# Performance work log

Measured on AMD Instinct MI355X. Metric: run time of the kernel, lower is better.

Reference implementation:

```python
import jax, jax.numpy as jnp
import numpy as np
import math

D_MODEL = 1024
N_HEADS = 16
HEAD_DIM = D_MODEL // N_HEADS
SEQ_LEN = 8192
INCLUDE_LOCAL = 2


def get_dilated_positions(seq_len, include_local=2):
    # Faithful numpy port of the torch pattern generator (runs once at setup).
    max_attend = include_local + int(math.ceil(math.log2(seq_len + 1)))
    positions = np.zeros((seq_len, max_attend), dtype=np.int64)
    mask = np.zeros((seq_len, max_attend), dtype=bool)
    for i in range(seq_len):
        ap = [i]
        for j in range(1, include_local + 1):
            if i - j >= 0:
                ap.append(i - j)
        k = 2
        while i - 2 ** k >= 0:
            ap.append(i - 2 ** k)
            k += 1
        positions[i, :len(ap)] = ap
        mask[i, :len(ap)] = True
    return positions, mask


def setup_inputs() -> dict:
    key = jax.random.key(0)
    kx, kq, kk, kv, ko = jax.random.split(key, 5)
    x = jax.random.normal(kx, (1, SEQ_LEN, D_MODEL), dtype=jnp.float32)
    # nn.Linear(bias=False) weights, torch layout [out_features, in_features]
    s = 0.02
    q_w = jax.random.normal(kq, (D_MODEL, D_MODEL), dtype=jnp.float32) * s
    k_w = jax.random.normal(kk, (D_MODEL, D_MODEL), dtype=jnp.float32) * s
    v_w = jax.random.normal(kv, (D_MODEL, D_MODEL), dtype=jnp.float32) * s
    o_w = jax.random.normal(ko, (D_MODEL, D_MODEL), dtype=jnp.float32) * s
    pos_np, mask_np = get_dilated_positions(SEQ_LEN, INCLUDE_LOCAL)
    return {
        "x": x,
        "q_w": q_w, "k_w": k_w, "v_w": v_w, "o_w": o_w,
        "positions": jnp.asarray(pos_np),   # (S, A) int64 indices
        "attend_mask": jnp.asarray(mask_np) # (S, A) bool
    }


def reference(x, q_w, k_w, v_w, o_w, positions, attend_mask):
    B, S, _ = x.shape
    H, Dh = N_HEADS, HEAD_DIM
    scale = Dh ** -0.5

    q = (x @ q_w.T).reshape(B, S, H, Dh).transpose(0, 2, 1, 3)  # (B,H,S,Dh)
    k = (x @ k_w.T).reshape(B, S, H, Dh).transpose(0, 2, 1, 3)
    v = (x @ v_w.T).reshape(B, S, H, Dh).transpose(0, 2, 1, 3)

    # Gather K/V at the dilated positions: (B,H,S,A,Dh)
    k_sparse = k[:, :, positions, :]
    v_sparse = v[:, :, positions, :]

    scores = jnp.einsum('bhsd,bhsad->bhsa', q, k_sparse) * scale
    scores = jnp.where(attend_mask[None, None, :, :], scores, -jnp.inf)
    attn = jax.nn.softmax(scores, axis=-1)  # dropout p in eval / 0.0 -> identity

    out = jnp.einsum('bhsa,bhsad->bhsd', attn, v_sparse)
    out = out.transpose(0, 2, 1, 3).reshape(B, S, D_MODEL)
    return out @ o_w.T
```

## Files before the change

### kernel.cpp

```cpp
#include <hip/hip_runtime.h>
#include <hip/hip_bf16.h>

typedef __bf16 bf16_t;
typedef __bf16 bf16x4 __attribute__((ext_vector_type(4)));
typedef __bf16 bf16x8 __attribute__((ext_vector_type(8)));
typedef float floatx16 __attribute__((ext_vector_type(16)));

#define SEQ    8192
#define DM     1024
#define NHEADS 16
#define HDIM   64

__device__ __forceinline__ void async_ld16(bf16_t* lds, const bf16_t* g) {
  __builtin_amdgcn_global_load_lds(
      (__attribute__((address_space(1))) void*)g,
      (__attribute__((address_space(3))) void*)lds, 16, 0, 0);
}

__global__ __launch_bounds__(256)
void cvt_all(const float* __restrict__ x,  const float* __restrict__ qw,
             const float* __restrict__ kw, const float* __restrict__ vw,
             const float* __restrict__ ow,
             bf16_t* __restrict__ Xb,  bf16_t* __restrict__ QWb,
             bf16_t* __restrict__ KWb, bf16_t* __restrict__ VWb,
             bf16_t* __restrict__ OWb) {
  const int b = blockIdx.x;
  const float* in; bf16_t* out; int g;
  if (b < 8192) { in = x; out = Xb; g = b; }
  else {
    const int w  = (b - 8192) >> 10;
    const int wb = (b - 8192) & 1023;
    switch (w) {
      case 0:  in = qw; out = QWb; break;
      case 1:  in = kw; out = KWb; break;
      case 2:  in = vw; out = VWb; break;
      default: in = ow; out = OWb; break;
    }
    g = wb;
  }
  const int idx = (g * 256 + threadIdx.x) * 4;
  float4 v = *(const float4*)(in + idx);
  bf16x4 o = { (bf16_t)v.x, (bf16_t)v.y, (bf16_t)v.z, (bf16_t)v.w };
  *(bf16x4*)(out + idx) = o;
}

template <typename OutT>
__device__ __forceinline__ void gemm128_core(
    const bf16_t* __restrict__ A, const bf16_t* __restrict__ B,
    OutT* __restrict__ C, float scl)
{
  constexpr int Kdim = DM;
  __shared__ __attribute__((aligned(16))) bf16_t sA[128 * 64];
  __shared__ __attribute__((aligned(16))) bf16_t sB[128 * 64];

  const int tid  = threadIdx.x;
  const int wave = tid >> 6;
  const int lane = tid & 63;
  const int l31  = lane & 31;
  const int half = lane >> 5;
  const int wr   = (wave >> 1) * 64;
  const int wc   = (wave & 1) * 64;

  const int gc = (lane & 7) ^ ((lane >> 3) & 7);
  const size_t arow0 = (size_t)blockIdx.x * 128 + wave * 32 + (lane >> 3);
  const size_t brow0 = (size_t)blockIdx.y * 128 + wave * 32 + (lane >> 3);
  const bf16_t* Ag = A + arow0 * Kdim + gc * 8;
  const bf16_t* Bg = B + brow0 * Kdim + gc * 8;
  bf16_t* sAw = sA + wave * 32 * 64;
  bf16_t* sBw = sB + wave * 32 * 64;

  floatx16 acc[2][2];
  #pragma unroll
  for (int i = 0; i < 2; ++i)
    #pragma unroll
    for (int j = 0; j < 2; ++j)
      acc[i][j] = (floatx16)(0.0f);

  const int sw = l31 & 7;

  for (int ko = 0; ko < Kdim; ko += 64) {
    #pragma unroll
    for (int n = 0; n < 4; ++n) {
      async_ld16(sAw + n * 512, Ag + (size_t)n * 8 * Kdim + ko);
      async_ld16(sBw + n * 512, Bg + (size_t)n * 8 * Kdim + ko);
    }
    __syncthreads();

    #pragma unroll
    for (int s = 0; s < 4; ++s) {
      const int ck   = s * 2 + half;
      const int slot = (ck ^ sw) * 8;
      bf16x8 af[2], bfr[2];
      #pragma unroll
      for (int mi = 0; mi < 2; ++mi)
        af[mi] = *(const bf16x8*)&sA[(wr + mi * 32 + l31) * 64 + slot];
      #pragma unroll
      for (int ni = 0; ni < 2; ++ni)
        bfr[ni] = *(const bf16x8*)&sB[(wc + ni * 32 + l31) * 64 + slot];

      #pragma unroll
      for (int mi = 0; mi < 2; ++mi)
        #pragma unroll
        for (int ni = 0; ni < 2; ++ni)
          acc[mi][ni] = __builtin_amdgcn_mfma_f32_32x32x16_bf16(af[mi], bfr[ni], acc[mi][ni], 0, 0, 0);
    }

    __syncthreads();
  }

  const int crow0 = blockIdx.x * 128 + wr + 4 * half;
  const int ccol0 = blockIdx.y * 128 + wc + l31;
  #pragma unroll
  for (int mi = 0; mi < 2; ++mi)
    #pragma unroll
    for (int ni = 0; ni < 2; ++ni)
      #pragma unroll
      for (int r = 0; r < 16; ++r) {
        const int row = crow0 + mi * 32 + (r & 3) + 8 * (r >> 2);
        C[(size_t)row * DM + (ccol0 + ni * 32)] = (OutT)(acc[mi][ni][r] * scl);
      }
}

__global__ __launch_bounds__(256)
void gemm_proj(const bf16_t* __restrict__ A, const bf16_t* __restrict__ B,
               bf16_t* __restrict__ C, float scl)
{
  gemm128_core<bf16_t>(A, B, C, scl);
}

__global__ __launch_bounds__(256)
void gemm_outk(const bf16_t* __restrict__ A, const bf16_t* __restrict__ B,
               float* __restrict__ C)
{
  gemm128_core<float>(A, B, C, 1.0f);
}

__global__ __launch_bounds__(256)
void dilated_attn(const bf16_t* __restrict__ Q, const bf16_t* __restrict__ K,
                  const bf16_t* __restrict__ V, bf16_t* O)
{
  const int lane = threadIdx.x & 63;
  const int wv   = threadIdx.x >> 6;
  const int bid  = blockIdx.x;
  const int jj   = bid >> 3;
  const int chunk= (bid & 7) + ((jj >> 6) << 3);
  const int i    = chunk * 256 + (jj & 63) * 4 + wv;
  const size_t base = (size_t)i * DM + lane * 16;

  bf16x8 q0 = *(const bf16x8*)(Q + base);
  bf16x8 q1 = *(const bf16x8*)(Q + base + 8);
  float qf[16];
  #pragma unroll
  for (int j = 0; j < 8; ++j) { qf[j] = (float)q0[j]; qf[j + 8] = (float)q1[j]; }

  const int npos = (i == 0) ? 1 : (33 - __builtin_clz((unsigned)i));
  auto pos_addr = [&](int t) -> size_t {
    const int off = (t == 0) ? 0 : (1 << (t - 1));
    return (size_t)(i - off) * DM + lane * 16;
  };
  auto ld_pos = [&](int t, bf16x8& k0, bf16x8& k1, bf16x8& v0, bf16x8& v1) {
    const size_t a = pos_addr(t);
    k0 = *(const bf16x8*)(K + a); k1 = *(const bf16x8*)(K + a + 8);
    v0 = *(const bf16x8*)(V + a); v1 = *(const bf16x8*)(V + a + 8);
  };

  float mE = -INFINITY, lE = 0.0f, mD = -INFINITY, lD = 0.0f;
  float aE[16], aD[16];
  #pragma unroll
  for (int j = 0; j < 16; ++j) { aE[j] = 0.0f; aD[j] = 0.0f; }

  auto step = [&](float& m, float& l, float* acc,
                  const bf16x8& k0, const bf16x8& k1,
                  const bf16x8& v0, const bf16x8& v1) {
    float sc = 0.0f;
    #pragma unroll
    for (int j = 0; j < 8; ++j) sc += qf[j] * (float)k0[j] + qf[j + 8] * (float)k1[j];
    sc += __shfl_xor(sc, 1, 64);
    sc += __shfl_xor(sc, 2, 64);
    const float mn = fmaxf(m, sc);
    const float co = __expf(m - mn);
    const float w  = __expf(sc - mn);
    l = l * co + w;
    m = mn;
    #pragma unroll
    for (int j = 0; j < 8; ++j) {
      acc[j]     = acc[j]     * co + w * (float)v0[j];
      acc[j + 8] = acc[j + 8] * co + w * (float)v1[j];
    }
  };

  bf16x8 xk0a, xk1a, xv0a, xv1a, xk0b, xk1b, xv0b, xv1b;
  bf16x8 yk0a, yk1a, yv0a, yv1a, yk0b, yk1b, yv0b, yv1b;

  ld_pos(0, xk0a, xk1a, xv0a, xv1a);
  if (1 < npos) ld_pos(1, xk0b, xk1b, xv0b, xv1b);

  for (int t = 0; ; t += 4) {
    const bool pe1 = (t + 2) < npos;
    if (pe1)            ld_pos(t + 2, yk0a, yk1a, yv0a, yv1a);
    const bool pd1 = (t + 3) < npos;
    if (pd1)            ld_pos(t + 3, yk0b, yk1b, yv0b, yv1b);
    step(mE, lE, aE, xk0a, xk1a, xv0a, xv1a);
    if ((t + 1) < npos) step(mD, lD, aD, xk0b, xk1b, xv0b, xv1b);
    if (!pe1) break;

    const bool pe2 = (t + 4) < npos;
    if (pe2)            ld_pos(t + 4, xk0a, xk1a, xv0a, xv1a);
    if ((t + 5) < npos) ld_pos(t + 5, xk0b, xk1b, xv0b, xv1b);
    step(mE, lE, aE, yk0a, yk1a, yv0a, yv1a);
    if (pd1)            step(mD, lD, aD, yk0b, yk1b, yv0b, yv1b);
    if (!pe2) break;
  }

  const float mt = fmaxf(mE, mD);
  const float ca = __expf(mE - mt);
  const float cb = __expf(mD - mt);
  const float inv = 1.0f / (lE * ca + lD * cb);
  bf16x8 o0, o1;
  #pragma unroll
  for (int j = 0; j < 8; ++j) {
    o0[j] = (bf16_t)((aE[j]     * ca + aD[j]     * cb) * inv);
    o1[j] = (bf16_t)((aE[j + 8] * ca + aD[j + 8] * cb) * inv);
  }
  *(bf16x8*)(O + base)     = o0;
  *(bf16x8*)(O + base + 8) = o1;
}

extern "C" void kernel_launch(void* const* d_in, const int* in_sizes, int n_in,
                              void* d_out, int out_size, void* d_ws, size_t ws_size,
                              hipStream_t stream) {
  (void)in_sizes; (void)n_in; (void)out_size; (void)ws_size;
  const float* x  = (const float*)d_in[0];
  const float* qw = (const float*)d_in[1];
  const float* kw = (const float*)d_in[2];
  const float* vw = (const float*)d_in[3];
  const float* ow = (const float*)d_in[4];
  float* out = (float*)d_out;

  bf16_t* Xb  = (bf16_t*)d_ws;
  bf16_t* Qb  = Xb  + (size_t)SEQ * DM;
  bf16_t* Kb  = Qb  + (size_t)SEQ * DM;
  bf16_t* Vb  = Kb  + (size_t)SEQ * DM;
  bf16_t* QWb = Vb  + (size_t)SEQ * DM;
  bf16_t* KWb = QWb + (size_t)DM * DM;
  bf16_t* VWb = KWb + (size_t)DM * DM;
  bf16_t* OWb = VWb + (size_t)DM * DM;
  bf16_t* AO  = Qb;

  cvt_all<<<dim3(8192 + 4096), dim3(256), 0, stream>>>(x, qw, kw, vw, ow,
                                                       Xb, QWb, KWb, VWb, OWb);

  dim3 pg(SEQ / 128, DM / 128);
  gemm_proj<<<pg, dim3(256), 0, stream>>>(Xb, QWb, Qb, 0.125f);
  gemm_proj<<<pg, dim3(256), 0, stream>>>(Xb, KWb, Kb, 1.0f);
  gemm_proj<<<pg, dim3(256), 0, stream>>>(Xb, VWb, Vb, 1.0f);
  dilated_attn<<<dim3(SEQ / 4), dim3(256), 0, stream>>>(Qb, Kb, Vb, AO);
  gemm_outk<<<pg, dim3(256), 0, stream>>>(AO, OWb, out);
}
```

Before: 224.2 us.

## Replace online softmax with fully unrolled two-pass softmax over fixed positions

```diff
diff --git a/kernel.cpp b/kernel.cpp
--- a/kernel.cpp
+++ b/kernel.cpp
@@ -154,73 +154,60 @@
   for (int j = 0; j < 8; ++j) { qf[j] = (float)q0[j]; qf[j + 8] = (float)q1[j]; }
 
   const int npos = (i == 0) ? 1 : (33 - __builtin_clz((unsigned)i));
-  auto pos_addr = [&](int t) -> size_t {
-    const int off = (t == 0) ? 0 : (1 << (t - 1));
-    return (size_t)(i - off) * DM + lane * 16;
-  };
-  auto ld_pos = [&](int t, bf16x8& k0, bf16x8& k1, bf16x8& v0, bf16x8& v1) {
-    const size_t a = pos_addr(t);
-    k0 = *(const bf16x8*)(K + a); k1 = *(const bf16x8*)(K + a + 8);
-    v0 = *(const bf16x8*)(V + a); v1 = *(const bf16x8*)(V + a + 8);
-  };
-
-  float mE = -INFINITY, lE = 0.0f, mD = -INFINITY, lD = 0.0f;
-  float aE[16], aD[16];
-  #pragma unroll
-  for (int j = 0; j < 16; ++j) { aE[j] = 0.0f; aD[j] = 0.0f; }
-
-  auto step = [&](float& m, float& l, float* acc,
-                  const bf16x8& k0, const bf16x8& k1,
-                  const bf16x8& v0, const bf16x8& v1) {
-    float sc = 0.0f;
-    #pragma unroll
-    for (int j = 0; j < 8; ++j) sc += qf[j] * (float)k0[j] + qf[j + 8] * (float)k1[j];
-    sc += __shfl_xor(sc, 1, 64);
-    sc += __shfl_xor(sc, 2, 64);
-    const float mn = fmaxf(m, sc);
-    const float co = __expf(m - mn);
-    const float w  = __expf(sc - mn);
-    l = l * co + w;
-    m = mn;
+
+  float sc[14];
+  #pragma unroll
+  for (int t = 0; t < 14; ++t) {
+    const size_t back = (t == 0) ? 0 : ((size_t)(1u << (t - 1)) * DM);
+    const size_t a = base - ((t < npos) ? back : 0);
+    const bf16x8 k0 = *(const bf16x8*)(K + a);
+    const bf16x8 k1 = *(const bf16x8*)(K + a + 8);
+    float s = 0.0f;
+    #pragma unroll
+    for (int j = 0; j < 8; ++j) s += qf[j] * (float)k0[j] + qf[j + 8] * (float)k1[j];
+    s += __shfl_xor(s, 1, 64);
+    s += __shfl_xor(s, 2, 64);
+    sc[t] = s;
+  }
+
+  float m01 = fmaxf(sc[0], sc[1]),  m23 = fmaxf(sc[2], sc[3]);
+  float m45 = fmaxf(sc[4], sc[5]),  m67 = fmaxf(sc[6], sc[7]);
+  float m89 = fmaxf(sc[8], sc[9]),  mab = fmaxf(sc[10], sc[11]);
+  float mcd = fmaxf(sc[12], sc[13]);
+  float m = fmaxf(fmaxf(fmaxf(m01, m23), fmaxf(m45, m67)),
+                  fmaxf(fmaxf(m89, mab), mcd));
+  float w[14];
+  #pragma unroll
+  for (int t = 0; t < 14; ++t) {
+    const float e = __expf(sc[t] - m);
+    w[t] = (t < npos) ? e : 0.0f;
+  }
+  float l01 = w[0]+w[1], l23 = w[2]+w[3], l45 = w[4]+w[5], l67 = w[6]+w[7];
+  float l89 = w[8]+w[9], lab = w[10]+w[11], lcd = w[12]+w[13];
+  const float l = ((l01+l23)+(l45+l67)) + ((l89+lab)+lcd);
+
+  float acc[16];
+  #pragma unroll
+  for (int j = 0; j < 16; ++j) acc[j] = 0.0f;
+  #pragma unroll
+  for (int t = 0; t < 14; ++t) {
+    const size_t back = (t == 0) ? 0 : ((size_t)(1u << (t - 1)) * DM);
+    const size_t a = base - ((t < npos) ? back : 0);
+    const bf16x8 v0 = *(const bf16x8*)(V + a);
+    const bf16x8 v1 = *(const bf16x8*)(V + a + 8);
     #pragma unroll
     for (int j = 0; j < 8; ++j) {
-      acc[j]     = acc[j]     * co + w * (float)v0[j];
-      acc[j + 8] = acc[j + 8] * co + w * (float)v1[j];
-    }
-  };
-
-  bf16x8 xk0a, xk1a, xv0a, xv1a, xk0b, xk1b, xv0b, xv1b;
-  bf16x8 yk0a, yk1a, yv0a, yv1a, yk0b, yk1b, yv0b, yv1b;
-
-  ld_pos(0, xk0a, xk1a, xv0a, xv1a);
-  if (1 < npos) ld_pos(1, xk0b, xk1b, xv0b, xv1b);
-
-  for (int t = 0; ; t += 4) {
-    const bool pe1 = (t + 2) < npos;
-    if (pe1)            ld_pos(t + 2, yk0a, yk1a, yv0a, yv1a);
-    const bool pd1 = (t + 3) < npos;
-    if (pd1)            ld_pos(t + 3, yk0b, yk1b, yv0b, yv1b);
-    step(mE, lE, aE, xk0a, xk1a, xv0a, xv1a);
-    if ((t + 1) < npos) step(mD, lD, aD, xk0b, xk1b, xv0b, xv1b);
-    if (!pe1) break;
-
-    const bool pe2 = (t + 4) < npos;
-    if (pe2)            ld_pos(t + 4, xk0a, xk1a, xv0a, xv1a);
-    if ((t + 5) < npos) ld_pos(t + 5, xk0b, xk1b, xv0b, xv1b);
-    step(mE, lE, aE, yk0a, yk1a, yv0a, yv1a);
-    if (pd1)            step(mD, lD, aD, yk0b, yk1b, yv0b, yv1b);
-    if (!pe2) break;
-  }
-
-  const float mt = fmaxf(mE, mD);
-  const float ca = __expf(mE - mt);
-  const float cb = __expf(mD - mt);
-  const float inv = 1.0f / (lE * ca + lD * cb);
+      acc[j]     += w[t] * (float)v0[j];
+      acc[j + 8] += w[t] * (float)v1[j];
+    }
+  }
+
+  const float inv = 1.0f / l;
   bf16x8 o0, o1;
   #pragma unroll
   for (int j = 0; j < 8; ++j) {
-    o0[j] = (bf16_t)((aE[j]     * ca + aD[j]     * cb) * inv);
-    o1[j] = (bf16_t)((aE[j + 8] * ca + aD[j + 8] * cb) * inv);
+    o0[j] = (bf16_t)(acc[j]     * inv);
+    o1[j] = (bf16_t)(acc[j + 8] * inv);
   }
   *(bf16x8*)(O + base)     = o0;
   *(bf16x8*)(O + base + 8) = o1;
```

Measured after the change: 229.9 us. +2.6%, slower.
